# Performance work log

Measured on AMD Instinct MI355X. Metric: run time of the kernel, lower is better.

Reference implementation:

```python
import jax, jax.numpy as jnp
import numpy as np

HEADS = 16
KV_HEADS = 4
HEAD_DIM = 64
HIDDEN = 1024
ROPE_THETA = 10000.0
NEG = -1e9


def _rope_cos_sin(seq_len, head_dim, dtype):
    inv_freq = 1.0 / (ROPE_THETA ** (jnp.arange(0, head_dim, 2, dtype=jnp.float32) / head_dim))
    pos = jnp.arange(seq_len, dtype=jnp.float32)
    freqs = jnp.outer(pos, inv_freq)                      # [S, d/2]
    emb = jnp.concatenate([freqs, freqs], axis=-1)        # [S, d]
    return jnp.cos(emb).astype(dtype), jnp.sin(emb).astype(dtype)


def _rotate_half(x):
    x1, x2 = jnp.split(x, 2, axis=-1)
    return jnp.concatenate([-x2, x1], axis=-1)


def setup_inputs() -> dict:
    key = jax.random.key(0)
    ks = jax.random.split(key, 5)
    B, S = 2, 2048
    hidden_states = jax.random.normal(ks[0], (B, S, HIDDEN), dtype=jnp.float32)
    # additive causal mask [1,1,S,S]
    causal = jnp.tril(jnp.ones((S, S), dtype=bool))
    attention_mask = jnp.where(causal, 0.0, NEG).astype(jnp.float32)[None, None]
    scale = 0.02
    Wq = jax.random.normal(ks[1], (HIDDEN, HEADS * HEAD_DIM), dtype=jnp.float32) * scale
    Wk = jax.random.normal(ks[2], (HIDDEN, KV_HEADS * HEAD_DIM), dtype=jnp.float32) * scale
    Wv = jax.random.normal(ks[3], (HIDDEN, KV_HEADS * HEAD_DIM), dtype=jnp.float32) * scale
    Wo = jax.random.normal(ks[4], (HEADS * HEAD_DIM, HIDDEN), dtype=jnp.float32) * scale
    return {"hidden_states": hidden_states, "attention_mask": attention_mask,
            "Wq": Wq, "Wk": Wk, "Wv": Wv, "Wo": Wo}


def reference(hidden_states, attention_mask, Wq, Wk, Wv, Wo):
    B, S, _ = hidden_states.shape
    G = HEADS // KV_HEADS  # kv groups

    q = (hidden_states @ Wq).reshape(B, S, HEADS, HEAD_DIM).transpose(0, 2, 1, 3)      # [B,H,S,d]
    k = (hidden_states @ Wk).reshape(B, S, KV_HEADS, HEAD_DIM).transpose(0, 2, 1, 3)   # [B,Hk,S,d]
    v = (hidden_states @ Wv).reshape(B, S, KV_HEADS, HEAD_DIM).transpose(0, 2, 1, 3)   # [B,Hk,S,d]

    cos, sin = _rope_cos_sin(S, HEAD_DIM, q.dtype)  # [S,d], broadcasts over B,H
    q = q * cos + _rotate_half(q) * sin
    k = k * cos + _rotate_half(k) * sin

    # GQA: query head h attends to kv head h // G (== repeat_interleave on kv heads)
    qg = q.reshape(B, KV_HEADS, G, S, HEAD_DIM)
    scores = jnp.einsum('bkgqd,bkld->bkgql', qg, k) / np.float32(np.sqrt(HEAD_DIM))  # [B,Hk,G,S,S]
    scores = scores + attention_mask[:, :, None, :, :]
    probs = jax.nn.softmax(scores.astype(jnp.float32), axis=-1).astype(q.dtype)
    out = jnp.einsum('bkgql,bkld->bkgqd', probs, v)            # [B,Hk,G,S,d]
    out = out.reshape(B, HEADS, S, HEAD_DIM).transpose(0, 2, 1, 3).reshape(B, S, HEADS * HEAD_DIM)
    return out @ Wo
```

## Files before the change

### kernel.cpp

```cpp
#include <hip/hip_runtime.h>
#include <hip/hip_bf16.h>
#include <math.h>

#define HEADS 16
#define KV_HEADS 4
#define HEAD_DIM 64
#define HIDDEN 1024
#define BATCH 2
#define SEQ 2048
#define ROWS (BATCH*SEQ)
#define NQKV (HEADS*HEAD_DIM + 2*KV_HEADS*HEAD_DIM)
#define QSCL 0.1803368867f

typedef float f32x4 __attribute__((ext_vector_type(4)));
typedef __bf16 bf16x8 __attribute__((ext_vector_type(8)));
typedef int int4v __attribute__((ext_vector_type(4)));

static __device__ __forceinline__ unsigned short f2bf(float f) {
    union { float f; unsigned int u; } v; v.f = f;
    unsigned int r = v.u + 0x7fffu + ((v.u >> 16) & 1u);
    return (unsigned short)(r >> 16);
}

#define GLOAD_LDS16(gaddr, laddr) \
    __builtin_amdgcn_global_load_lds( \
        (const __attribute__((address_space(1))) unsigned int*)(gaddr), \
        (__attribute__((address_space(3))) unsigned int*)(laddr), 16, 0, 0)

__global__ __launch_bounds__(256) void k_fprep(const float* __restrict__ hs,
                                               const float* __restrict__ Wq,
                                               const float* __restrict__ Wk,
                                               const float* __restrict__ Wv,
                                               const float* __restrict__ Wo,
                                               unsigned short* __restrict__ hsb,
                                               unsigned short* __restrict__ WqkvT,
                                               unsigned short* __restrict__ WoT,
                                               float* __restrict__ cosT,
                                               float* __restrict__ sinT) {
    __shared__ float tile[64][65];
    int bx = blockIdx.x;
    if (bx < 640) {
        const float* src; unsigned short* dst; int ld, n0, k0;
        if (bx < 384) {
            int tn = bx % 24, tk = bx / 24;
            n0 = tn * 64; k0 = tk * 64; dst = WqkvT;
            if (n0 < 1024)      { src = Wq + n0;          ld = 1024; }
            else if (n0 < 1280) { src = Wk + (n0 - 1024); ld = 256;  }
            else                { src = Wv + (n0 - 1280); ld = 256;  }
        } else {
            int i2 = bx - 384;
            int tn = i2 & 15, tk = i2 >> 4;
            n0 = tn * 64; k0 = tk * 64;
            src = Wo + n0; ld = 1024; dst = WoT;
        }
        int tx = threadIdx.x & 63, ty = threadIdx.x >> 6;
#pragma unroll
        for (int j = 0; j < 16; j++) {
            int k = j * 4 + ty;
            tile[k][tx] = src[(size_t)(k0 + k) * ld + tx];
        }
        __syncthreads();
#pragma unroll
        for (int j = 0; j < 16; j++) {
            int r = j * 4 + ty;
            dst[(size_t)(n0 + r) * 1024 + k0 + tx] = f2bf(tile[tx][r]);
        }
    } else {
        int idx = (bx - 640) * 256 + threadIdx.x;
        int stride = 384 * 256;
        for (int i = idx; i < ROWS * HIDDEN / 4; i += stride) {
            float4 v = ((const float4*)hs)[i];
            hsb[i*4+0] = f2bf(v.x); hsb[i*4+1] = f2bf(v.y);
            hsb[i*4+2] = f2bf(v.z); hsb[i*4+3] = f2bf(v.w);
        }
        for (int i = idx; i < SEQ * 32; i += stride) {
            int s = i >> 5, f = i & 31;
            float inv = powf(10000.0f, -(float)f / 32.0f);
            float ang = (float)s * inv;
            cosT[i] = cosf(ang); sinT[i] = sinf(ang);
        }
    }
}

template <bool BF16_OUT, bool ROPE>
__global__ __launch_bounds__(256) void k_gemm(const unsigned short* __restrict__ A,
                                              const unsigned short* __restrict__ Bt,
                                              void* __restrict__ Cv,
                                              const float* __restrict__ cosT,
                                              const float* __restrict__ sinT,
                                              int M, int N, int K) {
    __shared__ unsigned short lA[2][128*64];
    __shared__ unsigned short lB[2][128*64];
    const int tid = threadIdx.x;
    const int lane = tid & 63;
    const int wid = tid >> 6;
    const int wr = wid >> 1, wc = wid & 1;
    const int m0 = blockIdx.y * 128;
    const int n0 = blockIdx.x * 128;
    const int l15 = lane & 15, lq = lane >> 4;

    f32x4 acc[4][4];
#pragma unroll
    for (int i = 0; i < 4; i++)
#pragma unroll
        for (int j = 0; j < 4; j++) acc[i][j] = (f32x4){0.f,0.f,0.f,0.f};

#define STAGE_AB(buf, k0)                                                         \
    {                                                                             \
        _Pragma("unroll")                                                         \
        for (int it = 0; it < 4; ++it) {                                          \
            int c = tid + it * 256;                                               \
            int row = c >> 3, slot = c & 7;                                       \
            int gs = slot ^ (row & 7);                                            \
            GLOAD_LDS16(A + (size_t)(m0 + row) * K + (k0) + gs * 8,               \
                        (char*)lA[buf] + c * 16);                                 \
            GLOAD_LDS16(Bt + (size_t)(n0 + row) * K + (k0) + gs * 8,              \
                        (char*)lB[buf] + c * 16);                                 \
        }                                                                         \
    }

    STAGE_AB(0, 0);
    __syncthreads();
    int cur = 0;

    for (int k0 = 0; k0 < K; k0 += 64) {
        if (k0 + 64 < K) STAGE_AB(cur ^ 1, k0 + 64);
#pragma unroll
        for (int t = 0; t < 2; t++) {
            bf16x8 af[4], bfr[4];
#pragma unroll
            for (int i = 0; i < 4; i++) {
                int row = wr * 64 + i * 16 + l15;
                int slot = (t * 4 + lq) ^ (row & 7);
                af[i] = *(const bf16x8*)((const char*)lA[cur] + row * 128 + slot * 16);
            }
#pragma unroll
            for (int j = 0; j < 4; j++) {
                int row = wc * 64 + j * 16 + l15;
                int slot = (t * 4 + lq) ^ (row & 7);
                bfr[j] = *(const bf16x8*)((const char*)lB[cur] + row * 128 + slot * 16);
            }
#pragma unroll
            for (int i = 0; i < 4; i++)
#pragma unroll
                for (int j = 0; j < 4; j++)
                    acc[i][j] = __builtin_amdgcn_mfma_f32_16x16x32_bf16(af[i], bfr[j], acc[i][j], 0, 0, 0);
        }
        __syncthreads();
        cur ^= 1;
    }
#undef STAGE_AB
    if constexpr (ROPE) {
        const int hc0 = n0 + wc * 64;
        if (hc0 < 1280) {
            const float scl = (hc0 < 1024) ? QSCL : 1.0f;
#pragma unroll
            for (int i = 0; i < 4; i++) {
#pragma unroll
                for (int r = 0; r < 4; r++) {
                    int row = m0 + wr * 64 + i * 16 + lq * 4 + r;
                    int s = row & (SEQ - 1);
                    float c_lo = cosT[s * 32 + l15],      c_hi = cosT[s * 32 + 16 + l15];
                    float s_lo = sinT[s * 32 + l15],      s_hi = sinT[s * 32 + 16 + l15];
#pragma unroll
                    for (int j = 0; j < 4; j++) {
                        float c  = (j & 1) ? c_hi : c_lo;
                        float sn = (j & 1) ? s_hi : s_lo;
                        float v = acc[i][j][r], vp = acc[i][j ^ 2][r];
                        float o = (j < 2) ? (v * c - vp * sn) : (v * c + vp * sn);
                        int col = n0 + wc * 64 + j * 16 + l15;
                        ((unsigned short*)Cv)[(size_t)row * N + col] = f2bf(o * scl);
                    }
                }
            }
            return;
        }
    }
#pragma unroll
    for (int i = 0; i < 4; i++) {
#pragma unroll
        for (int j = 0; j < 4; j++) {
            int col = n0 + wc * 64 + j * 16 + l15;
#pragma unroll
            for (int r = 0; r < 4; r++) {
                int row = m0 + wr * 64 + i * 16 + lq * 4 + r;
                if constexpr (BF16_OUT)
                    ((unsigned short*)Cv)[(size_t)row * N + col] = f2bf(acc[i][j][r]);
                else
                    ((float*)Cv)[(size_t)row * N + col] = acc[i][j][r];
            }
        }
    }
}

__global__ __launch_bounds__(256) void k_vtrans(const unsigned short* __restrict__ QKVb,
                                                unsigned short* __restrict__ Vt) {
    __shared__ unsigned short tile[64][66];
    int s0 = blockIdx.x * 64;
    int bhk = blockIdx.y;
    int b = bhk >> 2, hk = bhk & 3;
    int t = threadIdx.x;
    int r = t >> 3, c = t & 7;
    const unsigned short* base = QKVb + (size_t)b * SEQ * NQKV + 1280 + hk * 64;
#pragma unroll
    for (int rr = r; rr < 64; rr += 32) {
        unsigned short tmp[8];
        *(int4v*)tmp = *(const int4v*)(base + (size_t)(s0 + rr) * NQKV + c * 8);
#pragma unroll
        for (int e = 0; e < 8; e++) tile[rr][c * 8 + e] = tmp[e];
    }
    __syncthreads();
    unsigned short* outb = Vt + (size_t)bhk * 64 * SEQ;
#pragma unroll
    for (int dd = r; dd < 64; dd += 32) {
        unsigned short tmp[8];
#pragma unroll
        for (int e = 0; e < 8; e++) tmp[e] = tile[c * 8 + e][dd];
        *(int4v*)(outb + (size_t)dd * SEQ + s0 + c * 8) = *(int4v*)tmp;
    }
}

__global__ __launch_bounds__(256) void k_attn(const unsigned short* __restrict__ QKVb,
                                              const unsigned short* __restrict__ Vt,
                                              unsigned short* __restrict__ Ob) {
    __shared__ unsigned short lK[2][64*64];
    __shared__ unsigned short lV[2][64*64];
    __shared__ unsigned short lP[4][16*64];
    const int tid = threadIdx.x;
    const int lane = tid & 63;
    const int w = tid >> 6;
    const int l15 = lane & 15, lq = lane >> 4;
    const int bh = blockIdx.x;
    const int qt = (int)gridDim.y - 1 - (int)blockIdx.y;
    const int b = bh >> 4, h = bh & 15;
    const int hk = h >> 2;
    const int q0 = qt * 64;

    bf16x8 aq[2];
    {
        int s = q0 + w * 16 + l15;
        const unsigned short* Qp = QKVb + (size_t)(b * SEQ + s) * NQKV + h * 64;
        aq[0] = *(const bf16x8*)(Qp + lq * 8);
        aq[1] = *(const bf16x8*)(Qp + 32 + lq * 8);
    }

    f32x4 oacc[4];
#pragma unroll
    for (int d = 0; d < 4; d++) oacc[d] = (f32x4){0.f,0.f,0.f,0.f};
    float mrun = -INFINITY, lrun = 0.f;

    const unsigned short* Kg = QKVb + (size_t)b * SEQ * NQKV + 1024 + hk * 64;
    const unsigned short* Vg = Vt + (size_t)(b * KV_HEADS + hk) * 64 * SEQ;

#define STAGE_KV(buf, kv0)                                                        \
    {                                                                             \
        _Pragma("unroll")                                                         \
        for (int it = 0; it < 2; ++it) {                                          \
            int c = tid + it * 256;                                               \
            int row = c >> 3, slot = c & 7;                                       \
            int gs = slot ^ (row & 7);                                            \
            GLOAD_LDS16(Kg + (size_t)((kv0) + row) * NQKV + gs * 8,               \
                        (char*)lK[buf] + c * 16);                                 \
            GLOAD_LDS16(Vg + (size_t)row * SEQ + (kv0) + gs * 8,                  \
                        (char*)lV[buf] + c * 16);                                 \
        }                                                                         \
    }

    STAGE_KV(0, 0);
    __syncthreads();
    int cur = 0;

    for (int j = 0; j <= qt; ++j) {
        if (j < qt) STAGE_KV(cur ^ 1, (j + 1) * 64);

        int kv0 = j * 64;
        f32x4 sT[4];
        __builtin_amdgcn_s_setprio(1);
#pragma unroll
        for (int kb = 0; kb < 4; kb++) {
            sT[kb] = (f32x4){0.f,0.f,0.f,0.f};
#pragma unroll
            for (int t = 0; t < 2; t++) {
                int row = kb * 16 + l15;
                int slot = (t * 4 + lq) ^ (row & 7);
                bf16x8 bk = *(const bf16x8*)((const char*)lK[cur] + row * 128 + slot * 16);
                sT[kb] = __builtin_amdgcn_mfma_f32_16x16x32_bf16(bk, aq[t], sT[kb], 0, 0, 0);
            }
        }
        __builtin_amdgcn_s_setprio(0);
        const int qg = q0 + w * 16 + l15;
        if (j == qt) {
#pragma unroll
            for (int kb = 0; kb < 4; kb++)
#pragma unroll
                for (int r = 0; r < 4; r++) {
                    int kvg = kv0 + kb * 16 + lq * 4 + r;
                    if (kvg > qg) sT[kb][r] = -INFINITY;
                }
        }
        float m;
        {
            f32x4 mx = sT[0];
#pragma unroll
            for (int kb = 1; kb < 4; kb++) {
#pragma unroll
                for (int r = 0; r < 4; r++) mx[r] = fmaxf(mx[r], sT[kb][r]);
            }
            m = fmaxf(fmaxf(mx[0], mx[1]), fmaxf(mx[2], mx[3]));
            m = fmaxf(m, __shfl_xor(m, 16));
            m = fmaxf(m, __shfl_xor(m, 32));
        }
        if (__any(m > mrun)) {
            float newm = fmaxf(mrun, m);
            float fac = exp2f(mrun - newm);
            mrun = newm;
            lrun *= fac;
#pragma unroll
            for (int r = 0; r < 4; r++) {
                float facr = __shfl(fac, (lane & 48) | (lq * 4 + r));
#pragma unroll
                for (int d = 0; d < 4; d++) oacc[d][r] *= facr;
            }
        }
        float rs = 0.f;
#pragma unroll
        for (int kb = 0; kb < 4; kb++)
#pragma unroll
            for (int r = 0; r < 4; r++) {
                float p = exp2f(sT[kb][r] - mrun);
                sT[kb][r] = p; rs += p;
            }
        rs += __shfl_xor(rs, 16);
        rs += __shfl_xor(rs, 32);
        lrun += rs;
        unsigned short* lPw = lP[w];
#pragma unroll
        for (int kb = 0; kb < 4; kb++)
#pragma unroll
            for (int r = 0; r < 4; r++) {
                int kv = kb * 16 + lq * 4 + r;
                int byte = (l15 * 128 + kv * 2) ^ ((l15 & 7) << 4);
                *(__bf16*)((char*)lPw + byte) = (__bf16)sT[kb][r];
            }
        __builtin_amdgcn_s_setprio(1);
#pragma unroll
        for (int t = 0; t < 2; t++) {
            int qr = l15;
            int slota = (t * 4 + lq) ^ (qr & 7);
            bf16x8 ap = *(const bf16x8*)((const char*)lPw + qr * 128 + slota * 16);
#pragma unroll
            for (int db = 0; db < 4; db++) {
                int vrow = db * 16 + l15;
                int slotv = (t * 4 + lq) ^ (vrow & 7);
                bf16x8 bv = *(const bf16x8*)((const char*)lV[cur] + vrow * 128 + slotv * 16);
                oacc[db] = __builtin_amdgcn_mfma_f32_16x16x32_bf16(ap, bv, oacc[db], 0, 0, 0);
            }
        }
        __builtin_amdgcn_s_setprio(0);
        __syncthreads();
        cur ^= 1;
    }
    float linvr[4];
#pragma unroll
    for (int r = 0; r < 4; r++)
        linvr[r] = 1.0f / __shfl(lrun, (lane & 48) | (lq * 4 + r));
#pragma unroll
    for (int db = 0; db < 4; db++)
#pragma unroll
        for (int r = 0; r < 4; r++) {
            int q = q0 + w * 16 + lq * 4 + r;
            int col = h * 64 + db * 16 + l15;
            Ob[((size_t)b * SEQ + q) * 1024 + col] = f2bf(oacc[db][r] * linvr[r]);
        }
#undef STAGE_KV
}

extern "C" void kernel_launch(void* const* d_in, const int* in_sizes, int n_in,
                              void* d_out, int out_size, void* d_ws, size_t ws_size,
                              hipStream_t stream) {
    const float* hs = (const float*)d_in[0];
    const float* Wq = (const float*)d_in[2];
    const float* Wk = (const float*)d_in[3];
    const float* Wv = (const float*)d_in[4];
    const float* Wo = (const float*)d_in[5];
    float* out = (float*)d_out;

    char* ws = (char*)d_ws;
    unsigned short* hsb   = (unsigned short*)ws; ws += (size_t)ROWS * HIDDEN * 2;
    unsigned short* WqkvT = (unsigned short*)ws; ws += (size_t)NQKV * HIDDEN * 2;
    unsigned short* WoT   = (unsigned short*)ws; ws += (size_t)HIDDEN * HIDDEN * 2;
    float* cosT = (float*)ws; ws += (size_t)SEQ * 32 * 4;
    float* sinT = (float*)ws; ws += (size_t)SEQ * 32 * 4;
    unsigned short* QKVb = (unsigned short*)ws; ws += (size_t)ROWS * NQKV * 2;
    unsigned short* Vt = (unsigned short*)ws; ws += (size_t)BATCH * KV_HEADS * 64 * SEQ * 2;
    unsigned short* Ob = (unsigned short*)ws; ws += (size_t)ROWS * HIDDEN * 2;

    k_fprep<<<1024, 256, 0, stream>>>(hs, Wq, Wk, Wv, Wo, hsb, WqkvT, WoT, cosT, sinT);

    dim3 g1(NQKV / 128, ROWS / 128);
    k_gemm<true, true><<<g1, 256, 0, stream>>>(hsb, WqkvT, QKVb, cosT, sinT, ROWS, NQKV, HIDDEN);

    k_vtrans<<<dim3(SEQ / 64, BATCH * KV_HEADS), 256, 0, stream>>>(QKVb, Vt);

    dim3 ga(BATCH * HEADS, SEQ / 64);
    k_attn<<<ga, 256, 0, stream>>>(QKVb, Vt, Ob);

    dim3 g2(HIDDEN / 128, ROWS / 128);
    k_gemm<false, false><<<g2, 256, 0, stream>>>(Ob, WoT, out, nullptr, nullptr, ROWS, HIDDEN, HIDDEN);
}
```

Before: 188.6 us.

## Shrink GEMM N-tile, swizzle block order, pass P via shuffles in attention

The GEMM tile shrinks from 128x128 to 128x64, so each wave owns 32 rows and twice as many blocks launch. Block indices are remapped with an XCD-style swizzle to improve L2 locality. Attention remaps blocks so the query heads sharing a KV head land together, and it moves the probability tile from an LDS round-trip into register cross-lane shuffles. The trade is more blocks and lower per-block reuse in the GEMMs, plus extra shuffle instructions in the attention inner loop.

```diff
diff --git a/kernel.cpp b/kernel.cpp
--- a/kernel.cpp
+++ b/kernel.cpp
@@ -90,18 +90,21 @@
                                               const float* __restrict__ sinT,
                                               int M, int N, int K) {
     __shared__ unsigned short lA[2][128*64];
-    __shared__ unsigned short lB[2][128*64];
+    __shared__ unsigned short lB[2][64*64];
     const int tid = threadIdx.x;
     const int lane = tid & 63;
-    const int wid = tid >> 6;
-    const int wr = wid >> 1, wc = wid & 1;
-    const int m0 = blockIdx.y * 128;
-    const int n0 = blockIdx.x * 128;
+    const int wr = tid >> 6;
+    const int gx = gridDim.x;
+    const int L = blockIdx.x + gx * blockIdx.y;
+    const int cpx = (gx * gridDim.y) >> 3;
+    const int swz = (L & 7) * cpx + (L >> 3);
+    const int m0 = (swz / gx) * 128;
+    const int n0 = (swz % gx) * 64;
     const int l15 = lane & 15, lq = lane >> 4;
 
-    f32x4 acc[4][4];
-#pragma unroll
-    for (int i = 0; i < 4; i++)
+    f32x4 acc[2][4];
+#pragma unroll
+    for (int i = 0; i < 2; i++)
 #pragma unroll
         for (int j = 0; j < 4; j++) acc[i][j] = (f32x4){0.f,0.f,0.f,0.f};
 
@@ -114,6 +117,12 @@
             int gs = slot ^ (row & 7);                                            \
             GLOAD_LDS16(A + (size_t)(m0 + row) * K + (k0) + gs * 8,               \
                         (char*)lA[buf] + c * 16);                                 \
+        }                                                                         \
+        _Pragma("unroll")                                                         \
+        for (int it = 0; it < 2; ++it) {                                          \
+            int c = tid + it * 256;                                               \
+            int row = c >> 3, slot = c & 7;                                       \
+            int gs = slot ^ (row & 7);                                            \
             GLOAD_LDS16(Bt + (size_t)(n0 + row) * K + (k0) + gs * 8,              \
                         (char*)lB[buf] + c * 16);                                 \
         }                                                                         \
@@ -127,21 +136,21 @@
         if (k0 + 64 < K) STAGE_AB(cur ^ 1, k0 + 64);
 #pragma unroll
         for (int t = 0; t < 2; t++) {
-            bf16x8 af[4], bfr[4];
-#pragma unroll
-            for (int i = 0; i < 4; i++) {
-                int row = wr * 64 + i * 16 + l15;
+            bf16x8 af[2], bfr[4];
+#pragma unroll
+            for (int i = 0; i < 2; i++) {
+                int row = wr * 32 + i * 16 + l15;
                 int slot = (t * 4 + lq) ^ (row & 7);
                 af[i] = *(const bf16x8*)((const char*)lA[cur] + row * 128 + slot * 16);
             }
 #pragma unroll
             for (int j = 0; j < 4; j++) {
-                int row = wc * 64 + j * 16 + l15;
+                int row = j * 16 + l15;
                 int slot = (t * 4 + lq) ^ (row & 7);
                 bfr[j] = *(const bf16x8*)((const char*)lB[cur] + row * 128 + slot * 16);
             }
 #pragma unroll
-            for (int i = 0; i < 4; i++)
+            for (int i = 0; i < 2; i++)
 #pragma unroll
                 for (int j = 0; j < 4; j++)
                     acc[i][j] = __builtin_amdgcn_mfma_f32_16x16x32_bf16(af[i], bfr[j], acc[i][j], 0, 0, 0);
@@ -151,14 +160,13 @@
     }
 #undef STAGE_AB
     if constexpr (ROPE) {
-        const int hc0 = n0 + wc * 64;
-        if (hc0 < 1280) {
-            const float scl = (hc0 < 1024) ? QSCL : 1.0f;
-#pragma unroll
-            for (int i = 0; i < 4; i++) {
+        if (n0 < 1280) {
+            const float scl = (n0 < 1024) ? QSCL : 1.0f;
+#pragma unroll
+            for (int i = 0; i < 2; i++) {
 #pragma unroll
                 for (int r = 0; r < 4; r++) {
-                    int row = m0 + wr * 64 + i * 16 + lq * 4 + r;
+                    int row = m0 + wr * 32 + i * 16 + lq * 4 + r;
                     int s = row & (SEQ - 1);
                     float c_lo = cosT[s * 32 + l15],      c_hi = cosT[s * 32 + 16 + l15];
                     float s_lo = sinT[s * 32 + l15],      s_hi = sinT[s * 32 + 16 + l15];
@@ -168,7 +176,7 @@
                         float sn = (j & 1) ? s_hi : s_lo;
                         float v = acc[i][j][r], vp = acc[i][j ^ 2][r];
                         float o = (j < 2) ? (v * c - vp * sn) : (v * c + vp * sn);
-                        int col = n0 + wc * 64 + j * 16 + l15;
+                        int col = n0 + j * 16 + l15;
                         ((unsigned short*)Cv)[(size_t)row * N + col] = f2bf(o * scl);
                     }
                 }
@@ -177,13 +185,13 @@
         }
     }
 #pragma unroll
-    for (int i = 0; i < 4; i++) {
+    for (int i = 0; i < 2; i++) {
 #pragma unroll
         for (int j = 0; j < 4; j++) {
-            int col = n0 + wc * 64 + j * 16 + l15;
+            int col = n0 + j * 16 + l15;
 #pragma unroll
             for (int r = 0; r < 4; r++) {
-                int row = m0 + wr * 64 + i * 16 + lq * 4 + r;
+                int row = m0 + wr * 32 + i * 16 + lq * 4 + r;
                 if constexpr (BF16_OUT)
                     ((unsigned short*)Cv)[(size_t)row * N + col] = f2bf(acc[i][j][r]);
                 else
@@ -225,15 +233,15 @@
                                               unsigned short* __restrict__ Ob) {
     __shared__ unsigned short lK[2][64*64];
     __shared__ unsigned short lV[2][64*64];
-    __shared__ unsigned short lP[4][16*64];
     const int tid = threadIdx.x;
     const int lane = tid & 63;
     const int w = tid >> 6;
     const int l15 = lane & 15, lq = lane >> 4;
-    const int bh = blockIdx.x;
-    const int qt = (int)gridDim.y - 1 - (int)blockIdx.y;
-    const int b = bh >> 4, h = bh & 15;
-    const int hk = h >> 2;
+    const int L = blockIdx.x + 32 * blockIdx.y;
+    const int b = (L >> 2) & 1;
+    const int hk = L & 3;
+    const int h = hk * 4 + ((L >> 3) & 3);
+    const int qt = 31 - (L >> 5);
     const int q0 = qt * 64;
 
     bf16x8 aq[2];
@@ -333,27 +341,36 @@
         rs += __shfl_xor(rs, 16);
         rs += __shfl_xor(rs, 32);
         lrun += rs;
-        unsigned short* lPw = lP[w];
+        int pk[4][2];
 #pragma unroll
         for (int kb = 0; kb < 4; kb++)
 #pragma unroll
-            for (int r = 0; r < 4; r++) {
-                int kv = kb * 16 + lq * 4 + r;
-                int byte = (l15 * 128 + kv * 2) ^ ((l15 & 7) << 4);
-                *(__bf16*)((char*)lPw + byte) = (__bf16)sT[kb][r];
+            for (int d = 0; d < 2; d++) {
+                __hip_bfloat162 bb = __float22bfloat162_rn(
+                    make_float2(sT[kb][2 * d], sT[kb][2 * d + 1]));
+                pk[kb][d] = *reinterpret_cast<int*>(&bb);
             }
         __builtin_amdgcn_s_setprio(1);
 #pragma unroll
         for (int t = 0; t < 2; t++) {
-            int qr = l15;
-            int slota = (t * 4 + lq) ^ (qr & 7);
-            bf16x8 ap = *(const bf16x8*)((const char*)lPw + qr * 128 + slota * 16);
+            const int srcLo = l15 + ((lq & 1) << 5);
+            const int srcHi = srcLo + 16;
+            union { int u[4]; bf16x8 v; } ap;
+#pragma unroll
+            for (int d = 0; d < 2; d++) {
+                int a0 = __shfl(pk[2 * t + 0][d], srcLo);
+                int a1 = __shfl(pk[2 * t + 1][d], srcLo);
+                ap.u[d] = (lq >> 1) ? a1 : a0;
+                int b0 = __shfl(pk[2 * t + 0][d], srcHi);
+                int b1 = __shfl(pk[2 * t + 1][d], srcHi);
+                ap.u[2 + d] = (lq >> 1) ? b1 : b0;
+            }
 #pragma unroll
             for (int db = 0; db < 4; db++) {
                 int vrow = db * 16 + l15;
                 int slotv = (t * 4 + lq) ^ (vrow & 7);
                 bf16x8 bv = *(const bf16x8*)((const char*)lV[cur] + vrow * 128 + slotv * 16);
-                oacc[db] = __builtin_amdgcn_mfma_f32_16x16x32_bf16(ap, bv, oacc[db], 0, 0, 0);
+                oacc[db] = __builtin_amdgcn_mfma_f32_16x16x32_bf16(ap.v, bv, oacc[db], 0, 0, 0);
             }
         }
         __builtin_amdgcn_s_setprio(0);
@@ -397,14 +414,14 @@
 
     k_fprep<<<1024, 256, 0, stream>>>(hs, Wq, Wk, Wv, Wo, hsb, WqkvT, WoT, cosT, sinT);
 
-    dim3 g1(NQKV / 128, ROWS / 128);
+    dim3 g1(NQKV / 64, ROWS / 128);
     k_gemm<true, true><<<g1, 256, 0, stream>>>(hsb, WqkvT, QKVb, cosT, sinT, ROWS, NQKV, HIDDEN);
 
     k_vtrans<<<dim3(SEQ / 64, BATCH * KV_HEADS), 256, 0, stream>>>(QKVb, Vt);
 
-    dim3 ga(BATCH * HEADS, SEQ / 64);
+    dim3 ga(32, 32);
     k_attn<<<ga, 256, 0, stream>>>(QKVb, Vt, Ob);
 
-    dim3 g2(HIDDEN / 128, ROWS / 128);
+    dim3 g2(HIDDEN / 64, ROWS / 128);
     k_gemm<false, false><<<g2, 256, 0, stream>>>(Ob, WoT, out, nullptr, nullptr, ROWS, HIDDEN, HIDDEN);
 }
```

Result: no change. 187.0 us (-0.9%).
